# Kernel optimization log

Hardware: AMD Instinct MI355X
Metric: run time of the kernel (lower is better)

The kernel has to match this reference:

```python
import jax, jax.numpy as jnp
import numpy as np

B, N, F, O = 2, 8192, 64, 64

def setup_inputs() -> dict:
    key = jax.random.key(0)
    k1, k2, k3, k4, k5 = jax.random.split(key, 5)
    x = jax.random.normal(k1, (B, N, F), dtype=jnp.float32)
    adj_w = jax.random.normal(k2, (2 * F,), dtype=jnp.float32) * (1.0 / np.sqrt(2 * F))
    adj_b = jax.random.normal(k3, (1,), dtype=jnp.float32)
    weight = jax.random.normal(k4, (F, O), dtype=jnp.float32) * (1.0 / np.sqrt(F))
    bias = jax.random.normal(k5, (O,), dtype=jnp.float32)
    return {"x": x, "adj_w": adj_w, "adj_b": adj_b, "weight": weight, "bias": bias}

def reference(x, adj_w, adj_b, weight, bias):
    # Original: tmp[b,i,j]=x[b,j]; cat(tmp, tmp.T) -> [x[b,j], x[b,i]] -> Linear(2F,1).
    # Algebraically separable: adj[b,i,j] = w_j . x[b,j] + w_i . x[b,i] + b
    Fdim = x.shape[-1]
    w_j, w_i = adj_w[:Fdim], adj_w[Fdim:]
    sj = jnp.einsum('bnf,f->bn', x, w_j)  # contribution of column node j
    si = jnp.einsum('bnf,f->bn', x, w_i)  # contribution of row node i
    adj = si[:, :, None] + sj[:, None, :] + adj_b[0]  # (B,N,N)
    out = jnp.einsum('bnf,fo->bno', x, weight)  # (B,N,O)
    deg_inv_sqrt = jnp.maximum(adj.sum(axis=-1), 1.0) ** -0.5  # clamp(min=1).pow(-0.5)
    adj = deg_inv_sqrt[:, :, None] * adj * deg_inv_sqrt[:, None, :]
    out = jnp.einsum('bij,bjo->bio', adj, out) + bias
    return jax.nn.relu(out)
```

## Files before the change

### kernel.cpp

```cpp
#include <hip/hip_runtime.h>


#define NN 8192
#define FF 64

using ull = unsigned long long;
#define TAG1 0x5A170B91u
#define TAG2 0xC3A5965Au

__device__ __forceinline__ ull devloadu64(const ull* p) {
    return __hip_atomic_load(p, __ATOMIC_RELAXED, __HIP_MEMORY_SCOPE_AGENT);
}
__device__ __forceinline__ void devstoreu64(ull* p, ull v) {
    __hip_atomic_store(p, v, __ATOMIC_RELAXED, __HIP_MEMORY_SCOPE_AGENT);
}
__device__ __forceinline__ bool tagok(ull v, unsigned tag) {
    return (((unsigned)(v >> 32)) ^ ((unsigned)v)) == tag;
}

__global__ __launch_bounds__(256) void fused_gcn(
    const float* __restrict__ x,
    const float* __restrict__ adj_w,
    const float* __restrict__ adj_b,
    const float* __restrict__ weight,
    const float* __restrict__ bias,
    ull* __restrict__ sjpair,
    ull* __restrict__ flagB,
    ull* __restrict__ pq2,
    float* __restrict__ out)
{
    __shared__ float wjs[FF], wis[FF];
    __shared__ float xs[64 * FF];
    __shared__ float wsh[64 * 64];
    __shared__ float sish[64], sjsh[64], dsh[64], sjdsh[64];
    __shared__ float pacc[256], qacc[256];
    __shared__ float ps[64], qs[64], Us[64], Vs[64];
    __shared__ float SjTs;

    const int tid = threadIdx.x;
    const int bid = blockIdx.x;
    const int batch = bid >> 7;
    const int rowbase = bid * 64;

    if (tid < 2 * FF) {
        float v = adj_w[tid];
        if (tid < FF) wjs[tid] = v; else wis[tid - FF] = v;
    }
    __syncthreads();

    const int q4 = tid & 15, rl = tid >> 4;
    float4 wjv = reinterpret_cast<const float4*>(wjs)[q4];
    float4 wiv = reinterpret_cast<const float4*>(wis)[q4];
    #pragma unroll
    for (int pass = 0; pass < 4; ++pass) {
        int r = pass * 16 + rl;
        float4 xv = reinterpret_cast<const float4*>(x + (size_t)(rowbase + r) * FF)[q4];
        reinterpret_cast<float4*>(xs)[r * 16 + q4] = xv;
        float a = xv.x * wjv.x + xv.y * wjv.y + xv.z * wjv.z + xv.w * wjv.w;
        float b = xv.x * wiv.x + xv.y * wiv.y + xv.z * wiv.z + xv.w * wiv.w;
        #pragma unroll
        for (int s = 8; s; s >>= 1) {
            a += __shfl_down(a, s, 16);
            b += __shfl_down(b, s, 16);
        }
        if (q4 == 0) { sjsh[r] = a; sish[r] = b; }
    }
    __syncthreads();

    if (tid < 64) {
        float a = sjsh[tid];
        #pragma unroll
        for (int s = 32; s; s >>= 1) a += __shfl_down(a, s, 64);
        if (tid == 0) {
            unsigned lo = __float_as_uint(a);
            devstoreu64(&sjpair[bid], ((ull)(lo ^ TAG1) << 32) | (ull)lo);
        }
        const ull* pb = sjpair + batch * 128;
        ull v1, v2;
        for (;;) {
            v1 = devloadu64(pb + tid);
            v2 = devloadu64(pb + 64 + tid);
            if (__all(tagok(v1, TAG1) && tagok(v2, TAG1))) break;
            __builtin_amdgcn_s_sleep(1);
        }
        float s = __uint_as_float((unsigned)v1) + __uint_as_float((unsigned)v2);
        #pragma unroll
        for (int m = 32; m; m >>= 1) s += __shfl_xor(s, m, 64);
        if (tid == 0) SjTs = s;
    } else {
        for (int i = tid - 64; i < 1024; i += 192)
            reinterpret_cast<float4*>(wsh)[i] =
                reinterpret_cast<const float4*>(weight)[i];
    }
    __syncthreads();

    float cadj = adj_b[0];
    if (tid < 64) {
        float d = rsqrtf(fmaxf(8192.f * (sish[tid] + cadj) + SjTs, 1.f));
        dsh[tid] = d;
        sjdsh[tid] = sjsh[tid] * d;
    }
    __syncthreads();
    const int f = tid & 63, g = tid >> 6;
    {
        float pa = 0.f, qa = 0.f;
        #pragma unroll
        for (int r = g; r < 64; r += 4) {
            float xv = xs[r * FF + f];
            pa += dsh[r] * xv;
            qa += sjdsh[r] * xv;
        }
        pacc[tid] = pa; qacc[tid] = qa;
    }
    __syncthreads();

    if (tid < 64) {
        float pv = pacc[tid] + pacc[tid + 64] + pacc[tid + 128] + pacc[tid + 192];
        float qv = qacc[tid] + qacc[tid + 64] + qacc[tid + 128] + qacc[tid + 192];
        devstoreu64(&pq2[bid * 64 + tid],
                    ((ull)__float_as_uint(qv) << 32) | (ull)__float_as_uint(pv));
        asm volatile("s_waitcnt vmcnt(0)" ::: "memory");
        if (tid == 0)
            devstoreu64(&flagB[bid],
                        ((ull)((unsigned)bid ^ TAG2) << 32) | (ull)(unsigned)bid);
    } else if (tid < 128) {
        const ull* fb = flagB + batch * 128;
        int l = tid - 64;
        for (;;) {
            ull a = devloadu64(fb + l);
            ull b = devloadu64(fb + 64 + l);
            if (__all(tagok(a, TAG2) && tagok(b, TAG2))) break;
            __builtin_amdgcn_s_sleep(1);
        }
    }
    __syncthreads();

    {
        float pa = 0.f, qa = 0.f;
        const ull* pb = pq2 + (size_t)batch * 128 * 64 + f;
        #pragma unroll 8
        for (int b2 = g; b2 < 128; b2 += 4) {
            ull v = devloadu64(pb + (size_t)b2 * 64);
            pa += __uint_as_float((unsigned)v);
            qa += __uint_as_float((unsigned)(v >> 32));
        }
        pacc[tid] = pa; qacc[tid] = qa;
    }
    __syncthreads();
    if (tid < 64) {
        ps[tid] = pacc[tid] + pacc[tid + 64] + pacc[tid + 128] + pacc[tid + 192];
        qs[tid] = qacc[tid] + qacc[tid + 64] + qacc[tid + 128] + qacc[tid + 192];
    }
    __syncthreads();

    {
        int half = tid >> 7, sel = (tid >> 6) & 1, o = tid & 63;
        const float* src = sel ? qs : ps;
        int k0 = half * 32;
        float s = 0.f;
        #pragma unroll
        for (int k = 0; k < 32; ++k) s += src[k0 + k] * wsh[(k0 + k) * 64 + o];
        pacc[tid] = s;
    }
    __syncthreads();
    if (tid < 128) {
        int sel = tid >> 6, o = tid & 63;
        (sel ? Vs : Us)[o] = pacc[tid] + pacc[tid + 128];
    }
    __syncthreads();

    float4 bv = reinterpret_cast<const float4*>(bias)[q4];
    float4 Uv = reinterpret_cast<const float4*>(Us)[q4];
    float4 Vv = reinterpret_cast<const float4*>(Vs)[q4];
    #pragma unroll
    for (int pass = 0; pass < 4; ++pass) {
        int r = pass * 16 + rl;
        float d = dsh[r];
        float a = d * (sish[r] + cadj);
        float4 o;
        o.x = fmaxf(a * Uv.x + d * Vv.x + bv.x, 0.f);
        o.y = fmaxf(a * Uv.y + d * Vv.y + bv.y, 0.f);
        o.z = fmaxf(a * Uv.z + d * Vv.z + bv.z, 0.f);
        o.w = fmaxf(a * Uv.w + d * Vv.w + bv.w, 0.f);
        reinterpret_cast<float4*>(out + (size_t)(rowbase + r) * FF)[q4] = o;
    }
}

extern "C" void kernel_launch(void* const* d_in, const int* in_sizes, int n_in,
                              void* d_out, int out_size, void* d_ws, size_t ws_size,
                              hipStream_t stream) {
    const float* x      = (const float*)d_in[0];
    const float* adj_w  = (const float*)d_in[1];
    const float* adj_b  = (const float*)d_in[2];
    const float* weight = (const float*)d_in[3];
    const float* bias   = (const float*)d_in[4];
    float* out = (float*)d_out;

    ull* sjpair = (ull*)d_ws;
    ull* flagB  = (ull*)((char*)d_ws + 2048);
    ull* pq2    = (ull*)((char*)d_ws + 4096);

    fused_gcn<<<256, 256, 0, stream>>>(x, adj_w, adj_b, weight, bias,
                                       sjpair, flagB, pq2, out);
}
```

Baseline: 76.64 us.

## Replace per-block all-gather of partial sums with two-level tree reduction

```diff
diff --git a/kernel.cpp b/kernel.cpp
--- a/kernel.cpp
+++ b/kernel.cpp
@@ -7,6 +7,7 @@
 using ull = unsigned long long;
 #define TAG1 0x5A170B91u
 #define TAG2 0xC3A5965Au
+#define TAG3 0x7E39D04Du
 
 __device__ __forceinline__ ull devloadu64(const ull* p) {
     return __hip_atomic_load(p, __ATOMIC_RELAXED, __HIP_MEMORY_SCOPE_AGENT);
@@ -16,6 +17,10 @@
 }
 __device__ __forceinline__ bool tagok(ull v, unsigned tag) {
     return (((unsigned)(v >> 32)) ^ ((unsigned)v)) == tag;
+}
+__device__ __forceinline__ ull tagpack(float v, unsigned tag) {
+    unsigned lo = __float_as_uint(v);
+    return ((ull)(lo ^ tag) << 32) | (ull)lo;
 }
 
 __global__ __launch_bounds__(256) void fused_gcn(
@@ -27,9 +32,10 @@
     ull* __restrict__ sjpair,
     ull* __restrict__ flagB,
     ull* __restrict__ pq2,
+    ull* __restrict__ pB,
+    ull* __restrict__ qB,
     float* __restrict__ out)
 {
-    __shared__ float wjs[FF], wis[FF];
     __shared__ float xs[64 * FF];
     __shared__ float wsh[64 * 64];
     __shared__ float sish[64], sjsh[64], dsh[64], sjdsh[64];
@@ -41,20 +47,19 @@
     const int bid = blockIdx.x;
     const int batch = bid >> 7;
     const int rowbase = bid * 64;
-
-    if (tid < 2 * FF) {
-        float v = adj_w[tid];
-        if (tid < FF) wjs[tid] = v; else wis[tid - FF] = v;
-    }
-    __syncthreads();
-
     const int q4 = tid & 15, rl = tid >> 4;
-    float4 wjv = reinterpret_cast<const float4*>(wjs)[q4];
-    float4 wiv = reinterpret_cast<const float4*>(wis)[q4];
+
+    const float4* xp = reinterpret_cast<const float4*>(x + (size_t)rowbase * FF);
+    float4 xr[4];
+    #pragma unroll
+    for (int pass = 0; pass < 4; ++pass) xr[pass] = xp[(pass * 16 + rl) * 16 + q4];
+    float4 wjv = reinterpret_cast<const float4*>(adj_w)[q4];
+    float4 wiv = reinterpret_cast<const float4*>(adj_w)[16 + q4];
+    float cadj = adj_b[0];
     #pragma unroll
     for (int pass = 0; pass < 4; ++pass) {
         int r = pass * 16 + rl;
-        float4 xv = reinterpret_cast<const float4*>(x + (size_t)(rowbase + r) * FF)[q4];
+        float4 xv = xr[pass];
         reinterpret_cast<float4*>(xs)[r * 16 + q4] = xv;
         float a = xv.x * wjv.x + xv.y * wjv.y + xv.z * wjv.z + xv.w * wjv.w;
         float b = xv.x * wiv.x + xv.y * wiv.y + xv.z * wiv.z + xv.w * wiv.w;
@@ -71,10 +76,7 @@
         float a = sjsh[tid];
         #pragma unroll
         for (int s = 32; s; s >>= 1) a += __shfl_down(a, s, 64);
-        if (tid == 0) {
-            unsigned lo = __float_as_uint(a);
-            devstoreu64(&sjpair[bid], ((ull)(lo ^ TAG1) << 32) | (ull)lo);
-        }
+        if (tid == 0) devstoreu64(&sjpair[bid], tagpack(a, TAG1));
         const ull* pb = sjpair + batch * 128;
         ull v1, v2;
         for (;;) {
@@ -94,7 +96,6 @@
     }
     __syncthreads();
 
-    float cadj = adj_b[0];
     if (tid < 64) {
         float d = rsqrtf(fmaxf(8192.f * (sish[tid] + cadj) + SjTs, 1.f));
         dsh[tid] = d;
@@ -123,33 +124,66 @@
         if (tid == 0)
             devstoreu64(&flagB[bid],
                         ((ull)((unsigned)bid ^ TAG2) << 32) | (ull)(unsigned)bid);
+    }
+    __syncthreads();
+
+    if ((bid & 7) == 0) {
+        int r = (bid >> 3) & 15;
+        int sb0 = r * 8 + g, sb1 = sb0 + 4;
+        const ull* fb = flagB + batch * 128;
+        ull t0, t1;
+        for (;;) {
+            t0 = devloadu64(fb + sb0);
+            t1 = devloadu64(fb + sb1);
+            if (tagok(t0, TAG2) && tagok(t1, TAG2)) break;
+            __builtin_amdgcn_s_sleep(1);
+        }
+        ull v0 = devloadu64(pq2 + (size_t)(batch * 128 + sb0) * 64 + f);
+        ull v1 = devloadu64(pq2 + (size_t)(batch * 128 + sb1) * 64 + f);
+        pacc[tid] = __uint_as_float((unsigned)v0) + __uint_as_float((unsigned)v1);
+        qacc[tid] = __uint_as_float((unsigned)(v0 >> 32)) +
+                    __uint_as_float((unsigned)(v1 >> 32));
+        __syncthreads();
+        if (tid < 64) {
+            float v = pacc[tid] + pacc[tid + 64] + pacc[tid + 128] + pacc[tid + 192];
+            devstoreu64(&pB[(batch * 16 + r) * 64 + tid], tagpack(v, TAG3));
+        } else if (tid < 128) {
+            int t = tid - 64;
+            float v = qacc[t] + qacc[t + 64] + qacc[t + 128] + qacc[t + 192];
+            devstoreu64(&qB[(batch * 16 + r) * 64 + t], tagpack(v, TAG3));
+        }
+        __syncthreads();
+    }
+
+    {
+        const ull* cp = pB + (size_t)batch * 16 * 64 + f;
+        const ull* cq = qB + (size_t)batch * 16 * 64 + f;
+        ull w0, w1, w2, w3, z0, z1, z2, z3;
+        for (;;) {
+            w0 = devloadu64(cp + g * 64);
+            w1 = devloadu64(cp + (g + 4) * 64);
+            w2 = devloadu64(cp + (g + 8) * 64);
+            w3 = devloadu64(cp + (g + 12) * 64);
+            z0 = devloadu64(cq + g * 64);
+            z1 = devloadu64(cq + (g + 4) * 64);
+            z2 = devloadu64(cq + (g + 8) * 64);
+            z3 = devloadu64(cq + (g + 12) * 64);
+            if (tagok(w0, TAG3) && tagok(w1, TAG3) && tagok(w2, TAG3) &&
+                tagok(w3, TAG3) && tagok(z0, TAG3) && tagok(z1, TAG3) &&
+                tagok(z2, TAG3) && tagok(z3, TAG3)) break;
+            __builtin_amdgcn_s_sleep(1);
+        }
+        pacc[tid] = __uint_as_float((unsigned)w0) + __uint_as_float((unsigned)w1) +
+                    __uint_as_float((unsigned)w2) + __uint_as_float((unsigned)w3);
+        qacc[tid] = __uint_as_float((unsigned)z0) + __uint_as_float((unsigned)z1) +
+                    __uint_as_float((unsigned)z2) + __uint_as_float((unsigned)z3);
+    }
+    __syncthreads();
+    if (tid < 64) {
+        ps[tid] = pacc[tid] + pacc[tid + 64] + pacc[tid + 128] + pacc[tid + 192];
     } else if (tid < 128) {
-        const ull* fb = flagB + batch * 128;
-        int l = tid - 64;
-        for (;;) {
-            ull a = devloadu64(fb + l);
-            ull b = devloadu64(fb + 64 + l);
-            if (__all(tagok(a, TAG2) && tagok(b, TAG2))) break;
-            __builtin_amdgcn_s_sleep(1);
-        }
-    }
-    __syncthreads();
-
-    {
-        float pa = 0.f, qa = 0.f;
-        const ull* pb = pq2 + (size_t)batch * 128 * 64 + f;
-        #pragma unroll 8
-        for (int b2 = g; b2 < 128; b2 += 4) {
-            ull v = devloadu64(pb + (size_t)b2 * 64);
-            pa += __uint_as_float((unsigned)v);
-            qa += __uint_as_float((unsigned)(v >> 32));
-        }
-        pacc[tid] = pa; qacc[tid] = qa;
-    }
-    __syncthreads();
-    if (tid < 64) {
-        ps[tid] = pacc[tid] + pacc[tid + 64] + pacc[tid + 128] + pacc[tid + 192];
-        qs[tid] = qacc[tid] + qacc[tid + 64] + qacc[tid + 128] + qacc[tid + 192];
+        int t = tid - 64;
+        qs[t] = qacc[t] + qacc[t + 64] + qacc[t + 128] + qacc[t + 192];
     }
     __syncthreads();
 
@@ -199,7 +233,9 @@
     ull* sjpair = (ull*)d_ws;
     ull* flagB  = (ull*)((char*)d_ws + 2048);
     ull* pq2    = (ull*)((char*)d_ws + 4096);
+    ull* pB     = (ull*)((char*)d_ws + 4096 + 131072);
+    ull* qB     = (ull*)((char*)d_ws + 4096 + 147456);
 
     fused_gcn<<<256, 256, 0, stream>>>(x, adj_w, adj_b, weight, bias,
-                                       sjpair, flagB, pq2, out);
-}
+                                       sjpair, flagB, pq2, pB, qB, out);
+}
```

New measurement: 70.47 us. -8.0%, faster.

## Replace all-block flag barrier with tagged partial sums and hierarchical reducer blocks

Applied to the files above, without the earlier changes.

```diff
diff --git a/kernel.cpp b/kernel.cpp
--- a/kernel.cpp
+++ b/kernel.cpp
@@ -6,7 +6,9 @@
 
 using ull = unsigned long long;
 #define TAG1 0x5A170B91u
-#define TAG2 0xC3A5965Au
+#define TAGP 0xA1B2C3D4u
+#define TAGQ 0x1F2E3D4Cu
+#define TAGU 0x9E8D7C6Bu
 
 __device__ __forceinline__ ull devloadu64(const ull* p) {
     return __hip_atomic_load(p, __ATOMIC_RELAXED, __HIP_MEMORY_SCOPE_AGENT);
@@ -16,6 +18,13 @@
 }
 __device__ __forceinline__ bool tagok(ull v, unsigned tag) {
     return (((unsigned)(v >> 32)) ^ ((unsigned)v)) == tag;
+}
+__device__ __forceinline__ ull tagpack(float v, unsigned tag) {
+    unsigned lo = __float_as_uint(v);
+    return ((ull)(lo ^ tag) << 32) | (ull)lo;
+}
+__device__ __forceinline__ float tagval(ull v) {
+    return __uint_as_float((unsigned)v);
 }
 
 __global__ __launch_bounds__(256) void fused_gcn(
@@ -25,11 +34,11 @@
     const float* __restrict__ weight,
     const float* __restrict__ bias,
     ull* __restrict__ sjpair,
-    ull* __restrict__ flagB,
-    ull* __restrict__ pq2,
+    ull* __restrict__ pP,
+    ull* __restrict__ pQ,
+    ull* __restrict__ uvB,
     float* __restrict__ out)
 {
-    __shared__ float wjs[FF], wis[FF];
     __shared__ float xs[64 * FF];
     __shared__ float wsh[64 * 64];
     __shared__ float sish[64], sjsh[64], dsh[64], sjdsh[64];
@@ -41,20 +50,19 @@
     const int bid = blockIdx.x;
     const int batch = bid >> 7;
     const int rowbase = bid * 64;
-
-    if (tid < 2 * FF) {
-        float v = adj_w[tid];
-        if (tid < FF) wjs[tid] = v; else wis[tid - FF] = v;
-    }
-    __syncthreads();
-
     const int q4 = tid & 15, rl = tid >> 4;
-    float4 wjv = reinterpret_cast<const float4*>(wjs)[q4];
-    float4 wiv = reinterpret_cast<const float4*>(wis)[q4];
+
+    const float4* xp = reinterpret_cast<const float4*>(x + (size_t)rowbase * FF);
+    float4 xr[4];
+    #pragma unroll
+    for (int pass = 0; pass < 4; ++pass) xr[pass] = xp[(pass * 16 + rl) * 16 + q4];
+    float4 wjv = reinterpret_cast<const float4*>(adj_w)[q4];
+    float4 wiv = reinterpret_cast<const float4*>(adj_w)[16 + q4];
+    float cadj = adj_b[0];
     #pragma unroll
     for (int pass = 0; pass < 4; ++pass) {
         int r = pass * 16 + rl;
-        float4 xv = reinterpret_cast<const float4*>(x + (size_t)(rowbase + r) * FF)[q4];
+        float4 xv = xr[pass];
         reinterpret_cast<float4*>(xs)[r * 16 + q4] = xv;
         float a = xv.x * wjv.x + xv.y * wjv.y + xv.z * wjv.z + xv.w * wjv.w;
         float b = xv.x * wiv.x + xv.y * wiv.y + xv.z * wiv.z + xv.w * wiv.w;
@@ -71,10 +79,7 @@
         float a = sjsh[tid];
         #pragma unroll
         for (int s = 32; s; s >>= 1) a += __shfl_down(a, s, 64);
-        if (tid == 0) {
-            unsigned lo = __float_as_uint(a);
-            devstoreu64(&sjpair[bid], ((ull)(lo ^ TAG1) << 32) | (ull)lo);
-        }
+        if (tid == 0) devstoreu64(&sjpair[bid], tagpack(a, TAG1));
         const ull* pb = sjpair + batch * 128;
         ull v1, v2;
         for (;;) {
@@ -83,7 +88,7 @@
             if (__all(tagok(v1, TAG1) && tagok(v2, TAG1))) break;
             __builtin_amdgcn_s_sleep(1);
         }
-        float s = __uint_as_float((unsigned)v1) + __uint_as_float((unsigned)v2);
+        float s = tagval(v1) + tagval(v2);
         #pragma unroll
         for (int m = 32; m; m >>= 1) s += __shfl_xor(s, m, 64);
         if (tid == 0) SjTs = s;
@@ -94,7 +99,6 @@
     }
     __syncthreads();
 
-    float cadj = adj_b[0];
     if (tid < 64) {
         float d = rsqrtf(fmaxf(8192.f * (sish[tid] + cadj) + SjTs, 1.f));
         dsh[tid] = d;
@@ -117,55 +121,82 @@
     if (tid < 64) {
         float pv = pacc[tid] + pacc[tid + 64] + pacc[tid + 128] + pacc[tid + 192];
         float qv = qacc[tid] + qacc[tid + 64] + qacc[tid + 128] + qacc[tid + 192];
-        devstoreu64(&pq2[bid * 64 + tid],
-                    ((ull)__float_as_uint(qv) << 32) | (ull)__float_as_uint(pv));
-        asm volatile("s_waitcnt vmcnt(0)" ::: "memory");
-        if (tid == 0)
-            devstoreu64(&flagB[bid],
-                        ((ull)((unsigned)bid ^ TAG2) << 32) | (ull)(unsigned)bid);
-    } else if (tid < 128) {
-        const ull* fb = flagB + batch * 128;
-        int l = tid - 64;
+        devstoreu64(&pP[bid * 64 + tid], tagpack(pv, TAGP));
+        devstoreu64(&pQ[bid * 64 + tid], tagpack(qv, TAGQ));
+    }
+    __syncthreads();
+
+    {
+        int local = bid & 127;
+        int r = local / 17;
+        if (local == r * 17) {
+            int sb = (batch << 7) + r * 16;
+            const ull* bp = pP + (size_t)sb * 64 + f;
+            const ull* bq = pQ + (size_t)sb * 64 + f;
+            ull a0, a1, a2, a3, b0, b1, b2, b3;
+            for (;;) {
+                a0 = devloadu64(bp + (g + 0) * 64);
+                a1 = devloadu64(bp + (g + 4) * 64);
+                a2 = devloadu64(bp + (g + 8) * 64);
+                a3 = devloadu64(bp + (g + 12) * 64);
+                b0 = devloadu64(bq + (g + 0) * 64);
+                b1 = devloadu64(bq + (g + 4) * 64);
+                b2 = devloadu64(bq + (g + 8) * 64);
+                b3 = devloadu64(bq + (g + 12) * 64);
+                if (tagok(a0, TAGP) && tagok(a1, TAGP) && tagok(a2, TAGP) &&
+                    tagok(a3, TAGP) && tagok(b0, TAGQ) && tagok(b1, TAGQ) &&
+                    tagok(b2, TAGQ) && tagok(b3, TAGQ)) break;
+                __builtin_amdgcn_s_sleep(1);
+            }
+            pacc[tid] = tagval(a0) + tagval(a1) + tagval(a2) + tagval(a3);
+            qacc[tid] = tagval(b0) + tagval(b1) + tagval(b2) + tagval(b3);
+            __syncthreads();
+            if (tid < 64) {
+                ps[tid] = pacc[tid] + pacc[tid + 64] + pacc[tid + 128] + pacc[tid + 192];
+            } else if (tid < 128) {
+                int t = tid - 64;
+                qs[t] = qacc[t] + qacc[t + 64] + qacc[t + 128] + qacc[t + 192];
+            }
+            __syncthreads();
+            {
+                int half = tid >> 7, sel = (tid >> 6) & 1, o = tid & 63;
+                const float* src = sel ? qs : ps;
+                int k0 = half * 32;
+                float s = 0.f;
+                #pragma unroll
+                for (int k = 0; k < 32; ++k)
+                    s += src[k0 + k] * wsh[(k0 + k) * 64 + o];
+                pacc[tid] = s;
+            }
+            __syncthreads();
+            if (tid < 128) {
+                float v = pacc[tid] + pacc[tid + 128];
+                devstoreu64(&uvB[((size_t)batch * 8 + r) * 128 + tid],
+                            tagpack(v, TAGU));
+            }
+            __syncthreads();
+        }
+    }
+
+    {
+        int o = tid & 127, h = tid >> 7;
+        const ull* ub = uvB + (size_t)batch * 8 * 128 + o;
+        ull w0, w1, w2, w3;
         for (;;) {
-            ull a = devloadu64(fb + l);
-            ull b = devloadu64(fb + 64 + l);
-            if (__all(tagok(a, TAG2) && tagok(b, TAG2))) break;
+            w0 = devloadu64(ub + (h * 4 + 0) * 128);
+            w1 = devloadu64(ub + (h * 4 + 1) * 128);
+            w2 = devloadu64(ub + (h * 4 + 2) * 128);
+            w3 = devloadu64(ub + (h * 4 + 3) * 128);
+            if (tagok(w0, TAGU) && tagok(w1, TAGU) &&
+                tagok(w2, TAGU) && tagok(w3, TAGU)) break;
             __builtin_amdgcn_s_sleep(1);
         }
-    }
-    __syncthreads();
-
-    {
-        float pa = 0.f, qa = 0.f;
-        const ull* pb = pq2 + (size_t)batch * 128 * 64 + f;
-        #pragma unroll 8
-        for (int b2 = g; b2 < 128; b2 += 4) {
-            ull v = devloadu64(pb + (size_t)b2 * 64);
-            pa += __uint_as_float((unsigned)v);
-            qa += __uint_as_float((unsigned)(v >> 32));
-        }
-        pacc[tid] = pa; qacc[tid] = qa;
-    }
-    __syncthreads();
-    if (tid < 64) {
-        ps[tid] = pacc[tid] + pacc[tid + 64] + pacc[tid + 128] + pacc[tid + 192];
-        qs[tid] = qacc[tid] + qacc[tid + 64] + qacc[tid + 128] + qacc[tid + 192];
-    }
-    __syncthreads();
-
-    {
-        int half = tid >> 7, sel = (tid >> 6) & 1, o = tid & 63;
-        const float* src = sel ? qs : ps;
-        int k0 = half * 32;
-        float s = 0.f;
-        #pragma unroll
-        for (int k = 0; k < 32; ++k) s += src[k0 + k] * wsh[(k0 + k) * 64 + o];
-        pacc[tid] = s;
+        pacc[tid] = tagval(w0) + tagval(w1) + tagval(w2) + tagval(w3);
     }
     __syncthreads();
     if (tid < 128) {
-        int sel = tid >> 6, o = tid & 63;
-        (sel ? Vs : Us)[o] = pacc[tid] + pacc[tid + 128];
+        float v = pacc[tid] + pacc[tid + 128];
+        ((tid >> 6) ? Vs : Us)[tid & 63] = v;
     }
     __syncthreads();
 
@@ -197,9 +228,10 @@
     float* out = (float*)d_out;
 
     ull* sjpair = (ull*)d_ws;
-    ull* flagB  = (ull*)((char*)d_ws + 2048);
-    ull* pq2    = (ull*)((char*)d_ws + 4096);
+    ull* pP     = (ull*)((char*)d_ws + 4096);
+    ull* pQ     = (ull*)((char*)d_ws + 4096 + 131072);
+    ull* uvB    = (ull*)((char*)d_ws + 4096 + 262144);
 
     fused_gcn<<<256, 256, 0, stream>>>(x, adj_w, adj_b, weight, bias,
-                                       sjpair, flagB, pq2, out);
-}
+                                       sjpair, pP, pQ, uvB, out);
+}
```

Result: faster. 69.65 us (-9.1%).
